# Performance work log

Hardware: AMD Instinct MI355X
Metric: run time of the kernel (lower is better)

The kernel has to match this reference:

```python
import jax, jax.numpy as jnp
import numpy as np

HIDDEN = 1024
N_HEADS = 16
HEAD_DIM = HIDDEN // N_HEADS  # 64; RoPE applied only to first HEAD_DIM channels (head 0)
NUM_BUCKETS = 32
MAX_DISTANCE = 128
MLP_HIDDEN = 4 * HIDDEN
B, N = 2, 2048


def _rotate_half(x):
    # interleaved pairs [a0,b0,a1,b1,...] -> [-b0,a0,-b1,a1,...]
    sh = x.shape
    xr = x.reshape(sh[:-1] + (sh[-1] // 2, 2))
    x1, x2 = xr[..., 0], xr[..., 1]
    return jnp.stack([-x2, x1], axis=-1).reshape(sh)


def _rel_bucket(n, num_buckets=NUM_BUCKETS, max_distance=MAX_DISTANCE):
    # bidirectional T5 bucketing
    ctx = jnp.arange(n)[:, None]
    mem = jnp.arange(n)[None, :]
    rp = mem - ctx  # [n, n]
    nb = num_buckets // 2
    buckets = jnp.where(rp > 0, nb, 0)
    rp = jnp.abs(rp)
    max_exact = nb // 2
    is_small = rp < max_exact
    log_ratio = jnp.log(jnp.maximum(rp, 1).astype(jnp.float32) / max_exact)
    rpl = max_exact + (log_ratio / np.log(max_distance / max_exact) * (nb - max_exact)).astype(jnp.int32)
    rpl = jnp.minimum(rpl, nb - 1)
    return buckets + jnp.where(is_small, rp, rpl)


def _ln(x, eps=1e-6):
    # LayerNorm without affine (DiT elementwise_affine=False)
    m = jnp.mean(x, axis=-1, keepdims=True)
    v = jnp.mean(jnp.square(x - m), axis=-1, keepdims=True)
    return (x - m) * jax.lax.rsqrt(v + eps)


def setup_inputs() -> dict:
    key = jax.random.key(0)
    ks = jax.random.split(key, 12)
    s = 0.02
    return {
        "x": jax.random.normal(ks[0], (B, N, HIDDEN), dtype=jnp.float32),
        "c": jax.random.normal(ks[1], (B, HIDDEN), dtype=jnp.float32),
        "w_ada": jax.random.normal(ks[2], (HIDDEN, 6 * HIDDEN), dtype=jnp.float32) * s,
        "b_ada": jnp.zeros((6 * HIDDEN,), dtype=jnp.float32),
        "w_qkv": jax.random.normal(ks[3], (HIDDEN, 3 * HIDDEN), dtype=jnp.float32) * s,
        "b_qkv": jnp.zeros((3 * HIDDEN,), dtype=jnp.float32),
        "w_out": jax.random.normal(ks[4], (HIDDEN, HIDDEN), dtype=jnp.float32) * s,
        "b_out": jnp.zeros((HIDDEN,), dtype=jnp.float32),
        "rel_table": jax.random.normal(ks[5], (NUM_BUCKETS, N_HEADS), dtype=jnp.float32) * s,
        "w_mlp1": jax.random.normal(ks[6], (HIDDEN, MLP_HIDDEN), dtype=jnp.float32) * s,
        "b_mlp1": jnp.zeros((MLP_HIDDEN,), dtype=jnp.float32),
        "w_mlp2": jax.random.normal(ks[7], (MLP_HIDDEN, HIDDEN), dtype=jnp.float32) * s,
        "b_mlp2": jnp.zeros((HIDDEN,), dtype=jnp.float32),
    }


def reference(x, c, w_ada, b_ada, w_qkv, b_qkv, w_out, b_out, rel_table,
              w_mlp1, b_mlp1, w_mlp2, b_mlp2):
    Bb, n, hid = x.shape
    hd = HEAD_DIM

    # AdaLN-Zero modulation params from conditioning
    mod = jax.nn.silu(c) @ w_ada + b_ada  # [B, 6*hid]
    sh_msa, sc_msa, g_msa, sh_mlp, sc_mlp, g_mlp = jnp.split(mod, 6, axis=-1)

    # --- attention branch ---
    h = _ln(x) * (1.0 + sc_msa[:, None, :]) + sh_msa[:, None, :]
    qkv = h @ w_qkv + b_qkv
    q, k, v = jnp.split(qkv, 3, axis=-1)  # each [B, N, hid]

    # partial RoPE: only first head_dim channels (head 0), interleaved-duplicated freqs
    t = jnp.arange(n, dtype=jnp.float32)
    inv_freq = 1.0 / (10000.0 ** (jnp.arange(0, hd, 2, dtype=jnp.float32) / hd))
    fr = t[:, None] * inv_freq[None, :]               # [N, hd/2]
    fr = jnp.stack([fr, fr], axis=-1).reshape(n, hd)  # [N, hd] interleaved dup
    cos, sin = jnp.cos(fr)[None], jnp.sin(fr)[None]

    def partial_rope(a):
        r, u = a[..., :hd], a[..., hd:]
        r = r * cos + _rotate_half(r) * sin
        return jnp.concatenate([r, u], axis=-1)

    q = partial_rope(q)
    k = partial_rope(k)

    qh = q.reshape(Bb, n, N_HEADS, hd)
    kh = k.reshape(Bb, n, N_HEADS, hd)
    vh = v.reshape(Bb, n, N_HEADS, hd)

    scores = jnp.einsum('bqhd,bkhd->bhqk', qh, kh) / np.float32(np.sqrt(hd))
    bias = rel_table[_rel_bucket(n)]                 # [N, N, H]
    scores = scores + jnp.transpose(bias, (2, 0, 1))[None]  # [1,H,N,N]
    attn = jax.nn.softmax(scores, axis=-1)
    ctxv = jnp.einsum('bhqk,bkhd->bqhd', attn, vh).reshape(Bb, n, hid)
    attn_out = ctxv @ w_out + b_out
    x = x + g_msa[:, None, :] * attn_out

    # --- MLP branch ---
    h2 = _ln(x) * (1.0 + sc_mlp[:, None, :]) + sh_mlp[:, None, :]
    m = jax.nn.gelu(h2 @ w_mlp1 + b_mlp1, approximate=True) @ w_mlp2 + b_mlp2
    return x + g_mlp[:, None, :] * m
```

## Files before the change

kernel.cpp:

```cpp
#include <hip/hip_runtime.h>
#include <hip/hip_bf16.h>

#define SEQ 2048

typedef float f32x4 __attribute__((ext_vector_type(4)));
typedef float f32x16 __attribute__((ext_vector_type(16)));
typedef short short8 __attribute__((ext_vector_type(8)));
typedef int int4v __attribute__((ext_vector_type(4)));

static __device__ __forceinline__ unsigned short f2bf(float f) {
  __hip_bfloat16 h = __float2bfloat16(f);
  unsigned short u;
  __builtin_memcpy(&u, &h, 2);
  return u;
}
static __device__ __forceinline__ float bf2f(unsigned short u) {
  __hip_bfloat16 h;
  __builtin_memcpy(&h, &u, 2);
  return __bfloat162float(h);
}
static __device__ __forceinline__ void gload16(const void* g, void* l) {
  __builtin_amdgcn_global_load_lds(
      (const __attribute__((address_space(1))) void*)g,
      (__attribute__((address_space(3))) void*)l, 16, 0, 0);
}
static __device__ __forceinline__ float gelu_t(float x) {
  float t = x * x;
  float z = x * fmaf(0.1029442695044937f, t, 2.3021181827964594f);
  return x * __builtin_amdgcn_rcpf(1.f + exp2f(-z));
}
static __device__ __forceinline__ unsigned int cvtpk(float lo, float hi) {
  unsigned int r;
  asm("v_cvt_pk_bf16_f32 %0, %1, %2" : "=v"(r) : "v"(lo), "v"(hi));
  return r;
}
static __device__ __forceinline__ void rope_pair(short8& v, int m, int i, float pos) {
  const float fr = exp2f(-(float)(2 * i) * (13.287712379549449f / 64.f));
  const float ang = pos * fr;
  const float sn = sinf(ang), cs = cosf(ang);
  const float x0 = bf2f((unsigned short)v[2 * m]);
  const float x1 = bf2f((unsigned short)v[2 * m + 1]);
  v[2 * m] = (short)f2bf(x0 * cs - x1 * sn);
  v[2 * m + 1] = (short)f2bf(x1 * cs + x0 * sn);
}


#define SOFTMAX_M0 16.0f
__global__ void prep_misc(const float* __restrict__ c, float* __restrict__ siluc,
                          const float* __restrict__ rel_table, float* __restrict__ brp) {
  const int bid = blockIdx.x, t = threadIdx.x;
  if (bid < 8) {
    int i = bid * 256 + t;
    float v = c[i];
    siluc[i] = v / (1.f + expf(-v));
  } else {
    int idx = (bid - 8) * 256 + t;
    int h = idx >> 12, pos = idx & 4095;
    int rp = pos - 2047;
    int bucket = rp > 0 ? 16 : 0;
    int a = rp < 0 ? -rp : rp;
    int bi;
    if (a < 8) {
      bi = a;
    } else {
      bi = 8 + (int)(logf((float)a / 8.f) / 2.772588722239781f * 8.f);
      if (bi > 15) bi = 15;
    }
    brp[idx] = rel_table[(bucket + bi) * 16 + h] * 1.4426950408889634f - SOFTMAX_M0;
  }
}

__global__ void mod_part_k(const float* __restrict__ siluc, const float* __restrict__ w_ada,
                           float* __restrict__ part) {
  int gid = blockIdx.x * 256 + threadIdx.x;
  int kc = gid / 12288;
  int idx = gid - kc * 12288;
  int b = idx / 6144;
  int j = idx - b * 6144;
  const float* cp = siluc + b * 1024 + kc * 64;
  const float* wp = w_ada + (size_t)kc * 64 * 6144 + j;
  float acc = 0.f;
#pragma unroll 8
  for (int k = 0; k < 64; ++k) acc += cp[k] * wp[(size_t)k * 6144];
  part[gid] = acc;
}

__global__ void mod_reduce_k(const float* __restrict__ part, const float* __restrict__ b_ada,
                             float* __restrict__ mod) {
  int idx = blockIdx.x * 256 + threadIdx.x;
  int j = idx % 6144;
  float a = b_ada[j];
#pragma unroll
  for (int kc = 0; kc < 16; ++kc) a += part[kc * 12288 + idx];
  mod[idx] = a;
}

__global__ void transpose_all(const float* __restrict__ w_qkv, const float* __restrict__ w_out,
                              const float* __restrict__ w_mlp1, const float* __restrict__ w_mlp2,
                              unsigned short* __restrict__ dq, unsigned short* __restrict__ dwo,
                              unsigned short* __restrict__ dm1, unsigned short* __restrict__ dm2) {
  __shared__ float tile[32][33];
  const int bid = blockIdx.x;
  const float* src;
  unsigned short* dst;
  int K, N, NT, r;
  if (bid < 3072) {
    src = w_qkv; dst = dq; K = 1024; N = 3072; NT = 96; r = bid;
  } else if (bid < 4096) {
    src = w_out; dst = dwo; K = 1024; N = 1024; NT = 32; r = bid - 3072;
  } else if (bid < 8192) {
    src = w_mlp1; dst = dm1; K = 1024; N = 4096; NT = 128; r = bid - 4096;
  } else {
    src = w_mlp2; dst = dm2; K = 4096; N = 1024; NT = 32; r = bid - 8192;
  }
  const int nt = r % NT, kt = r / NT;
  const int t = threadIdx.x;
  const int col = t & 31, r0 = t >> 5;
#pragma unroll
  for (int i = 0; i < 4; ++i) {
    int rr = r0 + i * 8;
    tile[rr][col] = src[(size_t)(kt * 32 + rr) * N + nt * 32 + col];
  }
  __syncthreads();
#pragma unroll
  for (int i = 0; i < 4; ++i) {
    int rr = r0 + i * 8;
    dst[(size_t)(nt * 32 + rr) * K + kt * 32 + col] = f2bf(tile[col][rr]);
  }
}

__global__ void ln_mod(const float* __restrict__ x, const float* __restrict__ mod,
                       unsigned short* __restrict__ out, int sh_off, int sc_off) {
  int row = blockIdx.x;
  int b = row >> 11;
  int t = threadIdx.x;
  const float4 v = ((const float4*)(x + (size_t)row * 1024))[t];
  float s1 = v.x + v.y + v.z + v.w;
  float s2 = v.x * v.x + v.y * v.y + v.z * v.z + v.w * v.w;
#pragma unroll
  for (int off = 32; off; off >>= 1) {
    s1 += __shfl_xor(s1, off);
    s2 += __shfl_xor(s2, off);
  }
  __shared__ float red[8];
  int w = t >> 6, lane = t & 63;
  if (lane == 0) { red[w] = s1; red[4 + w] = s2; }
  __syncthreads();
  s1 = red[0] + red[1] + red[2] + red[3];
  s2 = red[4] + red[5] + red[6] + red[7];
  float mean = s1 * (1.f / 1024.f);
  float var = s2 * (1.f / 1024.f) - mean * mean;
  float rstd = rsqrtf(var + 1e-6f);
  const float* mb = mod + (size_t)b * 6144;
  int col = t * 4;
  ushort4 o4;
  o4.x = f2bf((v.x - mean) * rstd * (1.f + mb[sc_off + col + 0]) + mb[sh_off + col + 0]);
  o4.y = f2bf((v.y - mean) * rstd * (1.f + mb[sc_off + col + 1]) + mb[sh_off + col + 1]);
  o4.z = f2bf((v.z - mean) * rstd * (1.f + mb[sc_off + col + 2]) + mb[sh_off + col + 2]);
  o4.w = f2bf((v.w - mean) * rstd * (1.f + mb[sc_off + col + 3]) + mb[sh_off + col + 3]);
  *((ushort4*)(out + (size_t)row * 1024 + col)) = o4;
}

__global__ void kvpack(const unsigned short* __restrict__ qkv, unsigned short* __restrict__ kpk,
                       unsigned short* __restrict__ vpk) {
  const int kt = blockIdx.x;
  const int bh = blockIdx.y;
  const int b = bh >> 4, h = bh & 15;
  const int t = threadIdx.x;
  const int s = t >> 6, lane = t & 63;
  const int l31 = lane & 31, hi = lane >> 5;
  const size_t outbase = ((size_t)(bh * 64 + kt) * 4 + s) * 512 + lane * 8;
  {
    const unsigned short* src =
        qkv + (size_t)(b * SEQ + kt * 32 + l31) * 3072 + 1024 + h * 64 + s * 16 + hi * 8;
    short8 kv = *(const short8*)src;
    if (h == 0) {
      const float pos = (float)(kt * 32 + l31);
      const int d0 = s * 16 + hi * 8;
#pragma unroll
      for (int m = 0; m < 4; ++m) rope_pair(kv, m, (d0 >> 1) + m, pos);
    }
    *(short8*)(kpk + outbase) = kv;
  }
  {
    const int krow = kt * 32 + (s & 1) * 16 + hi * 8;
    const int d = (s >> 1) * 32 + l31;
    const unsigned short* src = qkv + (size_t)(b * SEQ + krow) * 3072 + 2048 + h * 64 + d;
    unsigned short v[8];
#pragma unroll
    for (int j = 0; j < 8; ++j) v[j] = src[(size_t)j * 3072];
    *(short8*)(vpk + outbase) = *(const short8*)v;
  }
}

template <int MODE, int BM, int BN, int PIPE>
__global__ __launch_bounds__(256) void gemm_bt(
    const unsigned short* __restrict__ A, const unsigned short* __restrict__ Bt,
    const float* __restrict__ bias, void* __restrict__ outp, const float* __restrict__ res,
    const float* __restrict__ mod, int goff, int N, int K) {
  constexpr int NBUF = PIPE ? 2 : 1;
  __shared__ __align__(16) unsigned short a_lds[NBUF][BM * 64];
  __shared__ __align__(16) unsigned short b_lds[NBUF][BN * 64];
  constexpr int WM = BM / 2, WN = BN / 2;
  constexpr int MT = WM / 16, NT = WN / 16;
  const int t = threadIdx.x;
  const int lane = t & 63;
  const int l15 = lane & 15, l4 = lane >> 4;
  const int w = t >> 6;
  const int wr = w >> 1, wc = w & 1;
  const int gx = gridDim.x;
  const int nwg = gx * gridDim.y;
  int wg = blockIdx.y * gx + blockIdx.x;
  wg = (wg & 7) * (nwg >> 3) + (wg >> 3);
  const int by = wg / gx, bx = wg - by * gx;
  const int rowA0 = by * BM;
  const int rowB0 = bx * BN;
  const int wub = t & ~63;

  f32x4 acc[MT][NT];
#pragma unroll
  for (int m = 0; m < MT; ++m)
#pragma unroll
    for (int n = 0; n < NT; ++n) acc[m][n] = (f32x4){0.f, 0.f, 0.f, 0.f};

  auto stage = [&](int buf, int kt) {
#pragma unroll
    for (int rnd = 0; rnd < BM / 32; ++rnd) {
      const int idx = rnd * 256 + t;
      const int row = idx >> 3;
      const int cb = ((idx & 7) << 4) ^ ((row & 7) << 4);
      const char* sa = (const char*)(A + (size_t)(rowA0 + row) * K + kt) + cb;
      gload16(sa, (char*)(&a_lds[buf][0]) + (size_t)(rnd * 256 + wub) * 16);
    }
#pragma unroll
    for (int rnd = 0; rnd < BN / 32; ++rnd) {
      const int idx = rnd * 256 + t;
      const int row = idx >> 3;
      const int cb = ((idx & 7) << 4) ^ ((row & 7) << 4);
      const char* sb = (const char*)(Bt + (size_t)(rowB0 + row) * K + kt) + cb;
      gload16(sb, (char*)(&b_lds[buf][0]) + (size_t)(rnd * 256 + wub) * 16);
    }
  };

  auto compute = [&](int buf) {
#pragma unroll
    for (int kb = 0; kb < 2; ++kb) {
      short8 af[MT], bfr[NT];
#pragma unroll
      for (int m = 0; m < MT; ++m) {
        int row = wr * WM + m * 16 + l15;
        int cb = (kb * 64 + l4 * 16) ^ ((row & 7) << 4);
        af[m] = *(const short8*)((const char*)(&a_lds[buf][0]) + row * 128 + cb);
      }
#pragma unroll
      for (int n = 0; n < NT; ++n) {
        int row = wc * WN + n * 16 + l15;
        int cb = (kb * 64 + l4 * 16) ^ ((row & 7) << 4);
        bfr[n] = *(const short8*)((const char*)(&b_lds[buf][0]) + row * 128 + cb);
      }
      __builtin_amdgcn_s_setprio(1);
#pragma unroll
      for (int m = 0; m < MT; ++m)
#pragma unroll
        for (int n = 0; n < NT; ++n)
          acc[m][n] = __builtin_amdgcn_mfma_f32_16x16x32_bf16(af[m], bfr[n], acc[m][n], 0, 0, 0);
      __builtin_amdgcn_s_setprio(0);
    }
  };

  if (PIPE) {
    stage(0, 0);
    __syncthreads();
    int cur = 0;
    for (int kt = 0; kt < K; kt += 64) {
      if (kt + 64 < K) stage(cur ^ 1, kt + 64);
      compute(cur);
      __syncthreads();
      cur ^= 1;
    }
  } else {
    for (int kt = 0; kt < K; kt += 64) {
      stage(0, kt);
      __syncthreads();
      compute(0);
      __syncthreads();
    }
  }

#pragma unroll
  for (int n = 0; n < NT; ++n) {
    const int col = rowB0 + wc * WN + n * 16 + l15;
    const float bv = bias[col];
#pragma unroll
    for (int m = 0; m < MT; ++m) {
      const int row0 = rowA0 + wr * WM + m * 16 + l4 * 4;
#pragma unroll
      for (int r = 0; r < 4; ++r) {
        float v = acc[m][n][r] + bv;
        const size_t o = (size_t)(row0 + r) * N + col;
        if (MODE == 0) {
          ((unsigned short*)outp)[o] = f2bf(v);
        } else if (MODE == 1) {
          ((unsigned short*)outp)[o] = f2bf(gelu_t(v));
        } else {
          float g = mod[(size_t)((row0 + r) >> 11) * 6144 + goff + col];
          ((float*)outp)[o] = res[o] + g * v;
        }
      }
    }
  }
}

__global__ __launch_bounds__(256) void attn_k(const unsigned short* __restrict__ qkv,
                                              const unsigned short* __restrict__ kpk,
                                              const unsigned short* __restrict__ vpk,
                                              const float* __restrict__ brp_all,
                                              unsigned short* __restrict__ ctxv) {
  const int t = threadIdx.x;
  const int w = t >> 6;
  const int lane = t & 63;
  const int l31 = lane & 31;
  const int hi = lane >> 5;
  const int wg = blockIdx.x;
  const int xcd = wg & 7, idx = wg >> 3;
  const int bh = xcd * 4 + (idx >> 4);
  const int qt = idx & 15;
  const int b = bh >> 4, h = bh & 15;
  const int qw = qt * 128 + w * 32;
  const float SC = 0.125f * 1.4426950408889634f;
  const float* brp = brp_all + (size_t)h * 4096;

  short8 qfr[4];
  {
    const unsigned short* qrow = qkv + (size_t)(b * SEQ + qw + l31) * 3072 + h * 64 + hi * 8;
#pragma unroll
    for (int kk = 0; kk < 4; ++kk) qfr[kk] = *(const short8*)(qrow + kk * 16);
    if (h == 0) {
      const float pos = (float)(qw + l31);
#pragma unroll
      for (int kk = 0; kk < 4; ++kk) {
        const int d0 = kk * 16 + hi * 8;
#pragma unroll
        for (int m = 0; m < 4; ++m) rope_pair(qfr[kk], m, (d0 >> 1) + m, pos);
      }
    }
  }
  const float bfar_pos = brp[4095], bfar_neg = brp[0];
  const float* bql = brp + 2047 + 4 * hi - (qw + l31);

  short8 ones;
#pragma unroll
  for (int i = 0; i < 8; ++i) ones[i] = (short)0x3F80;

  const unsigned short* kp = kpk + ((size_t)(bh * 64)) * 2048 + lane * 8;
  const unsigned short* vp = vpk + ((size_t)(bh * 64)) * 2048 + lane * 8;

  short8 kfrA[4], vfrA[4], kfrB[4], vfrB[4];
#pragma unroll
  for (int s = 0; s < 4; ++s) {
    kfrA[s] = *(const short8*)(kp + s * 512);
    vfrA[s] = *(const short8*)(vp + s * 512);
  }
  kp += 2048;
  vp += 2048;

  f32x16 oacc0 = {}, oacc1 = {}, lacc = {};
  int kbase = 0;

#define ATTN_TILE(KF, VF, KFN, VFN)                                                       \
  do {                                                                                    \
    KFN[0] = *(const short8*)(kp);                                                        \
    KFN[1] = *(const short8*)(kp + 512);                                                  \
    KFN[2] = *(const short8*)(kp + 1024);                                                 \
    KFN[3] = *(const short8*)(kp + 1536);                                                 \
    VFN[0] = *(const short8*)(vp);                                                        \
    VFN[1] = *(const short8*)(vp + 512);                                                  \
    VFN[2] = *(const short8*)(vp + 1024);                                                 \
    VFN[3] = *(const short8*)(vp + 1536);                                                 \
    kp += 2048;                                                                           \
    vp += 2048;                                                                           \
    f32x16 sacc = {};                                                                     \
    sacc = __builtin_amdgcn_mfma_f32_32x32x16_bf16(KF[0], qfr[0], sacc, 0, 0, 0);         \
    sacc = __builtin_amdgcn_mfma_f32_32x32x16_bf16(KF[1], qfr[1], sacc, 0, 0, 0);         \
    sacc = __builtin_amdgcn_mfma_f32_32x32x16_bf16(KF[2], qfr[2], sacc, 0, 0, 0);         \
    sacc = __builtin_amdgcn_mfma_f32_32x32x16_bf16(KF[3], qfr[3], sacc, 0, 0, 0);         \
    float p[16];                                                                          \
    const int dd = kbase - qw;                                                            \
    if (dd >= 128 || dd <= -128) {                                                        \
      const float bf_ = (dd > 0) ? bfar_pos : bfar_neg;                                   \
      _Pragma("unroll") for (int r = 0; r < 16; ++r)                                      \
          p[r] = __builtin_amdgcn_exp2f(fmaf(sacc[r], SC, bf_));                          \
    } else {                                                                              \
      const float* bp = bql + kbase;                                                      \
      _Pragma("unroll") for (int r = 0; r < 16; ++r)                                      \
          p[r] = __builtin_amdgcn_exp2f(fmaf(sacc[r], SC, bp[(r & 3) + 8 * (r >> 2)]));   \
    }                                                                                     \
    unsigned int x0 = cvtpk(p[0], p[1]), x1 = cvtpk(p[2], p[3]);                          \
    unsigned int y0 = cvtpk(p[4], p[5]), y1 = cvtpk(p[6], p[7]);                          \
    asm("v_permlane32_swap_b32 %0, %1" : "+v"(x0), "+v"(y0));                             \
    asm("v_permlane32_swap_b32 %0, %1" : "+v"(x1), "+v"(y1));                             \
    unsigned int x2 = cvtpk(p[8], p[9]), x3 = cvtpk(p[10], p[11]);                        \
    unsigned int y2 = cvtpk(p[12], p[13]), y3 = cvtpk(p[14], p[15]);                      \
    asm("v_permlane32_swap_b32 %0, %1" : "+v"(x2), "+v"(y2));                             \
    asm("v_permlane32_swap_b32 %0, %1" : "+v"(x3), "+v"(y3));                             \
    int4v pi0 = {(int)x0, (int)x1, (int)y0, (int)y1};                                     \
    int4v pi1 = {(int)x2, (int)x3, (int)y2, (int)y3};                                     \
    short8 pf0 = __builtin_bit_cast(short8, pi0);                                         \
    short8 pf1 = __builtin_bit_cast(short8, pi1);                                         \
    lacc = __builtin_amdgcn_mfma_f32_32x32x16_bf16(ones, pf0, lacc, 0, 0, 0);             \
    lacc = __builtin_amdgcn_mfma_f32_32x32x16_bf16(ones, pf1, lacc, 0, 0, 0);             \
    oacc0 = __builtin_amdgcn_mfma_f32_32x32x16_bf16(VF[0], pf0, oacc0, 0, 0, 0);          \
    oacc0 = __builtin_amdgcn_mfma_f32_32x32x16_bf16(VF[1], pf1, oacc0, 0, 0, 0);          \
    oacc1 = __builtin_amdgcn_mfma_f32_32x32x16_bf16(VF[2], pf0, oacc1, 0, 0, 0);          \
    oacc1 = __builtin_amdgcn_mfma_f32_32x32x16_bf16(VF[3], pf1, oacc1, 0, 0, 0);          \
    kbase += 32;                                                                          \
  } while (0)

#pragma unroll 1
  for (int it = 0; it < 32; ++it) {
    ATTN_TILE(kfrA, vfrA, kfrB, vfrB);
    ATTN_TILE(kfrB, vfrB, kfrA, vfrA);
  }
#undef ATTN_TILE

  const float inv = 1.f / lacc[0];
  unsigned short* orow = ctxv + (size_t)(b * SEQ + qw + l31) * 1024 + h * 64;
#pragma unroll
  for (int r = 0; r < 16; r += 2) {
    const int d = (r & 3) + 8 * (r >> 2) + 4 * hi;
    *(unsigned int*)(orow + d) = cvtpk(oacc0[r] * inv, oacc0[r + 1] * inv);
    *(unsigned int*)(orow + 32 + d) = cvtpk(oacc1[r] * inv, oacc1[r + 1] * inv);
  }
}

extern "C" void kernel_launch(void* const* d_in, const int* in_sizes, int n_in, void* d_out,
                              int out_size, void* d_ws, size_t ws_size, hipStream_t stream) {
  (void)in_sizes; (void)n_in; (void)out_size; (void)ws_size;
  const float* x = (const float*)d_in[0];
  const float* c = (const float*)d_in[1];
  const float* w_ada = (const float*)d_in[2];
  const float* b_ada = (const float*)d_in[3];
  const float* w_qkv = (const float*)d_in[4];
  const float* b_qkv = (const float*)d_in[5];
  const float* w_out = (const float*)d_in[6];
  const float* b_out = (const float*)d_in[7];
  const float* rel_t = (const float*)d_in[8];
  const float* w_mlp1 = (const float*)d_in[9];
  const float* b_mlp1 = (const float*)d_in[10];
  const float* w_mlp2 = (const float*)d_in[11];
  const float* b_mlp2 = (const float*)d_in[12];
  float* out = (float*)d_out;
  char* ws = (char*)d_ws;

  constexpr size_t OFF_WQKVT = 0;
  constexpr size_t OFF_WOUTT = OFF_WQKVT + (size_t)3072 * 1024 * 2;
  constexpr size_t OFF_WM1T = OFF_WOUTT + (size_t)1024 * 1024 * 2;
  constexpr size_t OFF_WM2T = OFF_WM1T + (size_t)4096 * 1024 * 2;
  constexpr size_t OFF_H = OFF_WM2T + (size_t)1024 * 4096 * 2;
  constexpr size_t OFF_QKV = OFF_H + (size_t)4096 * 1024 * 2;
  constexpr size_t OFF_VT = OFF_QKV + (size_t)4096 * 3072 * 2;
  constexpr size_t OFF_CTXV = OFF_VT + (size_t)32 * 64 * 2048 * 2;
  constexpr size_t OFF_MID = OFF_CTXV + (size_t)4096 * 1024 * 2;
  constexpr size_t OFF_SILU = OFF_MID + (size_t)4096 * 4096 * 2;
  constexpr size_t OFF_MOD = OFF_SILU + 2048 * 4;
  constexpr size_t OFF_BRP = OFF_MOD + 12288 * 4;
  constexpr size_t OFF_PART = OFF_BRP + 65536 * 4;

  unsigned short* wqkvT = (unsigned short*)(ws + OFF_WQKVT);
  unsigned short* woutT = (unsigned short*)(ws + OFF_WOUTT);
  unsigned short* wm1T = (unsigned short*)(ws + OFF_WM1T);
  unsigned short* wm2T = (unsigned short*)(ws + OFF_WM2T);
  unsigned short* hbuf = (unsigned short*)(ws + OFF_H);
  unsigned short* qkvbuf = (unsigned short*)(ws + OFF_QKV);
  unsigned short* vpkbuf = (unsigned short*)(ws + OFF_VT);
  unsigned short* ctxvbuf = (unsigned short*)(ws + OFF_CTXV);
  unsigned short* midbuf = (unsigned short*)(ws + OFF_MID);
  unsigned short* kpkbuf = (unsigned short*)(ws + OFF_MID);
  float* siluc = (float*)(ws + OFF_SILU);
  float* modb = (float*)(ws + OFF_MOD);
  float* brp = (float*)(ws + OFF_BRP);
  float* part = (float*)(ws + OFF_PART);

  prep_misc<<<264, 256, 0, stream>>>(c, siluc, rel_t, brp);
  mod_part_k<<<768, 256, 0, stream>>>(siluc, w_ada, part);
  mod_reduce_k<<<48, 256, 0, stream>>>(part, b_ada, modb);
  transpose_all<<<12288, 256, 0, stream>>>(w_qkv, w_out, w_mlp1, w_mlp2, wqkvT, woutT, wm1T,
                                           wm2T);

  ln_mod<<<4096, 256, 0, stream>>>(x, modb, hbuf, 0, 1024);
  gemm_bt<0, 128, 128, 0><<<dim3(24, 32), 256, 0, stream>>>(hbuf, wqkvT, b_qkv, qkvbuf, nullptr,
                                                            nullptr, 0, 3072, 1024);
  kvpack<<<dim3(64, 32), 256, 0, stream>>>(qkvbuf, kpkbuf, vpkbuf);
  attn_k<<<512, 256, 0, stream>>>(qkvbuf, kpkbuf, vpkbuf, brp, ctxvbuf);
  gemm_bt<2, 64, 64, 1><<<dim3(16, 64), 256, 0, stream>>>(ctxvbuf, woutT, b_out, out, x, modb,
                                                          2048, 1024, 1024);
  ln_mod<<<4096, 256, 0, stream>>>(out, modb, hbuf, 3072, 4096);
  gemm_bt<1, 128, 128, 0><<<dim3(32, 32), 256, 0, stream>>>(hbuf, wm1T, b_mlp1, midbuf, nullptr,
                                                            nullptr, 0, 4096, 1024);
  gemm_bt<2, 64, 64, 1><<<dim3(16, 64), 256, 0, stream>>>(midbuf, wm2T, b_mlp2, out, out, modb,
                                                          5120, 1024, 4096);
}
```

Baseline: 255.5 us.

## Fuse K/V packing into QKV GEMM epilogue and merge prep kernels

The QKV GEMM gets a new epilogue mode that scatters K and V directly into the packed attention layouts, so the separate kvpack kernel no longer re-reads the QKV buffer. RoPE on head 0 of K is applied by a small in-place krope_fix kernel. The prep_misc and transpose_all kernels are merged into one launch to save a kernel launch. The cost is scattered, uncoalesced 2-byte stores in the GEMM epilogue, which may slow that GEMM.

```diff
diff --git a/kernel.cpp b/kernel.cpp
--- a/kernel.cpp
+++ b/kernel.cpp
@@ -46,27 +46,62 @@
 
 
 #define SOFTMAX_M0 16.0f
-__global__ void prep_misc(const float* __restrict__ c, float* __restrict__ siluc,
-                          const float* __restrict__ rel_table, float* __restrict__ brp) {
-  const int bid = blockIdx.x, t = threadIdx.x;
-  if (bid < 8) {
-    int i = bid * 256 + t;
-    float v = c[i];
-    siluc[i] = v / (1.f + expf(-v));
+__global__ void prep_transpose(const float* __restrict__ w_qkv, const float* __restrict__ w_out,
+                               const float* __restrict__ w_mlp1, const float* __restrict__ w_mlp2,
+                               unsigned short* __restrict__ dq, unsigned short* __restrict__ dwo,
+                               unsigned short* __restrict__ dm1, unsigned short* __restrict__ dm2,
+                               const float* __restrict__ c, float* __restrict__ siluc,
+                               const float* __restrict__ rel_table, float* __restrict__ brp) {
+  const int bid = blockIdx.x;
+  const int t = threadIdx.x;
+  if (bid >= 12288) {
+    const int pb = bid - 12288;
+    if (pb < 8) {
+      int i = pb * 256 + t;
+      float v = c[i];
+      siluc[i] = v / (1.f + expf(-v));
+    } else {
+      int idx = (pb - 8) * 256 + t;
+      int h = idx >> 12, pos = idx & 4095;
+      int rp = pos - 2047;
+      int bucket = rp > 0 ? 16 : 0;
+      int a = rp < 0 ? -rp : rp;
+      int bi;
+      if (a < 8) {
+        bi = a;
+      } else {
+        bi = 8 + (int)(logf((float)a / 8.f) / 2.772588722239781f * 8.f);
+        if (bi > 15) bi = 15;
+      }
+      brp[idx] = rel_table[(bucket + bi) * 16 + h] * 1.4426950408889634f - SOFTMAX_M0;
+    }
+    return;
+  }
+  __shared__ float tile[32][33];
+  const float* src;
+  unsigned short* dst;
+  int K, N, NT, r;
+  if (bid < 3072) {
+    src = w_qkv; dst = dq; K = 1024; N = 3072; NT = 96; r = bid;
+  } else if (bid < 4096) {
+    src = w_out; dst = dwo; K = 1024; N = 1024; NT = 32; r = bid - 3072;
+  } else if (bid < 8192) {
+    src = w_mlp1; dst = dm1; K = 1024; N = 4096; NT = 128; r = bid - 4096;
   } else {
-    int idx = (bid - 8) * 256 + t;
-    int h = idx >> 12, pos = idx & 4095;
-    int rp = pos - 2047;
-    int bucket = rp > 0 ? 16 : 0;
-    int a = rp < 0 ? -rp : rp;
-    int bi;
-    if (a < 8) {
-      bi = a;
-    } else {
-      bi = 8 + (int)(logf((float)a / 8.f) / 2.772588722239781f * 8.f);
-      if (bi > 15) bi = 15;
-    }
-    brp[idx] = rel_table[(bucket + bi) * 16 + h] * 1.4426950408889634f - SOFTMAX_M0;
+    src = w_mlp2; dst = dm2; K = 4096; N = 1024; NT = 32; r = bid - 8192;
+  }
+  const int nt = r % NT, kt = r / NT;
+  const int col = t & 31, r0 = t >> 5;
+#pragma unroll
+  for (int i = 0; i < 4; ++i) {
+    int rr = r0 + i * 8;
+    tile[rr][col] = src[(size_t)(kt * 32 + rr) * N + nt * 32 + col];
+  }
+  __syncthreads();
+#pragma unroll
+  for (int i = 0; i < 4; ++i) {
+    int rr = r0 + i * 8;
+    dst[(size_t)(nt * 32 + rr) * K + kt * 32 + col] = f2bf(tile[col][rr]);
   }
 }
 
@@ -93,40 +128,6 @@
 #pragma unroll
   for (int kc = 0; kc < 16; ++kc) a += part[kc * 12288 + idx];
   mod[idx] = a;
-}
-
-__global__ void transpose_all(const float* __restrict__ w_qkv, const float* __restrict__ w_out,
-                              const float* __restrict__ w_mlp1, const float* __restrict__ w_mlp2,
-                              unsigned short* __restrict__ dq, unsigned short* __restrict__ dwo,
-                              unsigned short* __restrict__ dm1, unsigned short* __restrict__ dm2) {
-  __shared__ float tile[32][33];
-  const int bid = blockIdx.x;
-  const float* src;
-  unsigned short* dst;
-  int K, N, NT, r;
-  if (bid < 3072) {
-    src = w_qkv; dst = dq; K = 1024; N = 3072; NT = 96; r = bid;
-  } else if (bid < 4096) {
-    src = w_out; dst = dwo; K = 1024; N = 1024; NT = 32; r = bid - 3072;
-  } else if (bid < 8192) {
-    src = w_mlp1; dst = dm1; K = 1024; N = 4096; NT = 128; r = bid - 4096;
-  } else {
-    src = w_mlp2; dst = dm2; K = 4096; N = 1024; NT = 32; r = bid - 8192;
-  }
-  const int nt = r % NT, kt = r / NT;
-  const int t = threadIdx.x;
-  const int col = t & 31, r0 = t >> 5;
-#pragma unroll
-  for (int i = 0; i < 4; ++i) {
-    int rr = r0 + i * 8;
-    tile[rr][col] = src[(size_t)(kt * 32 + rr) * N + nt * 32 + col];
-  }
-  __syncthreads();
-#pragma unroll
-  for (int i = 0; i < 4; ++i) {
-    int rr = r0 + i * 8;
-    dst[(size_t)(nt * 32 + rr) * K + kt * 32 + col] = f2bf(tile[col][rr]);
-  }
 }
 
 __global__ void ln_mod(const float* __restrict__ x, const float* __restrict__ mod,
@@ -161,43 +162,32 @@
   *((ushort4*)(out + (size_t)row * 1024 + col)) = o4;
 }
 
-__global__ void kvpack(const unsigned short* __restrict__ qkv, unsigned short* __restrict__ kpk,
-                       unsigned short* __restrict__ vpk) {
-  const int kt = blockIdx.x;
-  const int bh = blockIdx.y;
-  const int b = bh >> 4, h = bh & 15;
-  const int t = threadIdx.x;
-  const int s = t >> 6, lane = t & 63;
-  const int l31 = lane & 31, hi = lane >> 5;
-  const size_t outbase = ((size_t)(bh * 64 + kt) * 4 + s) * 512 + lane * 8;
-  {
-    const unsigned short* src =
-        qkv + (size_t)(b * SEQ + kt * 32 + l31) * 3072 + 1024 + h * 64 + s * 16 + hi * 8;
-    short8 kv = *(const short8*)src;
-    if (h == 0) {
-      const float pos = (float)(kt * 32 + l31);
-      const int d0 = s * 16 + hi * 8;
-#pragma unroll
-      for (int m = 0; m < 4; ++m) rope_pair(kv, m, (d0 >> 1) + m, pos);
-    }
-    *(short8*)(kpk + outbase) = kv;
-  }
-  {
-    const int krow = kt * 32 + (s & 1) * 16 + hi * 8;
-    const int d = (s >> 1) * 32 + l31;
-    const unsigned short* src = qkv + (size_t)(b * SEQ + krow) * 3072 + 2048 + h * 64 + d;
-    unsigned short v[8];
-#pragma unroll
-    for (int j = 0; j < 8; ++j) v[j] = src[(size_t)j * 3072];
-    *(short8*)(vpk + outbase) = *(const short8*)v;
-  }
+__global__ void krope_fix(unsigned short* __restrict__ kpk) {
+  const int gid = blockIdx.x * 256 + threadIdx.x;
+  const int i = gid & 31;
+  const int l31 = (gid >> 5) & 31;
+  const int kt = (gid >> 10) & 63;
+  const int b = gid >> 16;
+  const int d = 2 * i;
+  const int bh = b * 16;
+  const size_t addr = (((size_t)(bh * 64 + kt) * 4 + (d >> 4)) * 512) +
+                      (((d >> 3) & 1) * 32 + l31) * 8 + (d & 7);
+  unsigned int pv = *(unsigned int*)(kpk + addr);
+  const float x0 = bf2f((unsigned short)(pv & 0xFFFF));
+  const float x1 = bf2f((unsigned short)(pv >> 16));
+  const float fr = exp2f(-(float)d * (13.287712379549449f / 64.f));
+  const float ang = (float)(kt * 32 + l31) * fr;
+  const float sn = sinf(ang), cs = cosf(ang);
+  *(unsigned int*)(kpk + addr) =
+      (unsigned int)f2bf(x0 * cs - x1 * sn) | ((unsigned int)f2bf(x1 * cs + x0 * sn) << 16);
 }
 
 template <int MODE, int BM, int BN, int PIPE>
 __global__ __launch_bounds__(256) void gemm_bt(
     const unsigned short* __restrict__ A, const unsigned short* __restrict__ Bt,
     const float* __restrict__ bias, void* __restrict__ outp, const float* __restrict__ res,
-    const float* __restrict__ mod, int goff, int N, int K) {
+    const float* __restrict__ mod, int goff, int N, int K,
+    unsigned short* __restrict__ kpkp, unsigned short* __restrict__ vpkp) {
   constexpr int NBUF = PIPE ? 2 : 1;
   __shared__ __align__(16) unsigned short a_lds[NBUF][BM * 64];
   __shared__ __align__(16) unsigned short b_lds[NBUF][BN * 64];
@@ -297,14 +287,37 @@
 #pragma unroll
       for (int r = 0; r < 4; ++r) {
         float v = acc[m][n][r] + bv;
-        const size_t o = (size_t)(row0 + r) * N + col;
         if (MODE == 0) {
-          ((unsigned short*)outp)[o] = f2bf(v);
+          ((unsigned short*)outp)[(size_t)(row0 + r) * N + col] = f2bf(v);
         } else if (MODE == 1) {
-          ((unsigned short*)outp)[o] = f2bf(gelu_t(v));
-        } else {
+          ((unsigned short*)outp)[(size_t)(row0 + r) * N + col] = f2bf(gelu_t(v));
+        } else if (MODE == 2) {
+          const size_t o = (size_t)(row0 + r) * N + col;
           float g = mod[(size_t)((row0 + r) >> 11) * 6144 + goff + col];
           ((float*)outp)[o] = res[o] + g * v;
+        } else {
+          const int rr = row0 + r;
+          if (rowB0 < 1024) {
+            ((unsigned short*)outp)[(size_t)rr * N + col] = f2bf(v);
+          } else if (rowB0 < 2048) {
+            const int bb = rr >> 11, krow = rr & 2047;
+            const int colk = col - 1024;
+            const int hh = colk >> 6, d = colk & 63;
+            const int bh2 = bb * 16 + hh;
+            const size_t addr = (((size_t)(bh2 * 64 + (krow >> 5)) * 4 + (d >> 4)) * 512) +
+                                (((d >> 3) & 1) * 32 + (krow & 31)) * 8 + (d & 7);
+            kpkp[addr] = f2bf(v);
+          } else {
+            const int bb = rr >> 11, krow = rr & 2047;
+            const int colv = col - 2048;
+            const int hh = colv >> 6, d = colv & 63;
+            const int bh2 = bb * 16 + hh;
+            const int r5 = krow & 31;
+            const int f = (d >> 5) * 2 + (r5 >> 4);
+            const size_t addr = (((size_t)(bh2 * 64 + (krow >> 5)) * 4 + f) * 512) +
+                                (((r5 >> 3) & 1) * 32 + (d & 31)) * 8 + (r5 & 7);
+            vpkp[addr] = f2bf(v);
+          }
         }
       }
     }
@@ -481,22 +494,23 @@
   float* brp = (float*)(ws + OFF_BRP);
   float* part = (float*)(ws + OFF_PART);
 
-  prep_misc<<<264, 256, 0, stream>>>(c, siluc, rel_t, brp);
+  prep_transpose<<<12552, 256, 0, stream>>>(w_qkv, w_out, w_mlp1, w_mlp2, wqkvT, woutT, wm1T,
+                                            wm2T, c, siluc, rel_t, brp);
   mod_part_k<<<768, 256, 0, stream>>>(siluc, w_ada, part);
   mod_reduce_k<<<48, 256, 0, stream>>>(part, b_ada, modb);
-  transpose_all<<<12288, 256, 0, stream>>>(w_qkv, w_out, w_mlp1, w_mlp2, wqkvT, woutT, wm1T,
-                                           wm2T);
 
   ln_mod<<<4096, 256, 0, stream>>>(x, modb, hbuf, 0, 1024);
-  gemm_bt<0, 128, 128, 0><<<dim3(24, 32), 256, 0, stream>>>(hbuf, wqkvT, b_qkv, qkvbuf, nullptr,
-                                                            nullptr, 0, 3072, 1024);
-  kvpack<<<dim3(64, 32), 256, 0, stream>>>(qkvbuf, kpkbuf, vpkbuf);
+  gemm_bt<3, 128, 128, 0><<<dim3(24, 32), 256, 0, stream>>>(hbuf, wqkvT, b_qkv, qkvbuf, nullptr,
+                                                            nullptr, 0, 3072, 1024, kpkbuf,
+                                                            vpkbuf);
+  krope_fix<<<512, 256, 0, stream>>>(kpkbuf);
   attn_k<<<512, 256, 0, stream>>>(qkvbuf, kpkbuf, vpkbuf, brp, ctxvbuf);
   gemm_bt<2, 64, 64, 1><<<dim3(16, 64), 256, 0, stream>>>(ctxvbuf, woutT, b_out, out, x, modb,
-                                                          2048, 1024, 1024);
+                                                          2048, 1024, 1024, nullptr, nullptr);
   ln_mod<<<4096, 256, 0, stream>>>(out, modb, hbuf, 3072, 4096);
   gemm_bt<1, 128, 128, 0><<<dim3(32, 32), 256, 0, stream>>>(hbuf, wm1T, b_mlp1, midbuf, nullptr,
-                                                            nullptr, 0, 4096, 1024);
+                                                            nullptr, 0, 4096, 1024, nullptr,
+                                                            nullptr);
   gemm_bt<2, 64, 64, 1><<<dim3(16, 64), 256, 0, stream>>>(midbuf, wm2T, b_mlp2, out, out, modb,
-                                                          5120, 1024, 4096);
-}
+                                                          5120, 1024, 4096, nullptr, nullptr);
+}
```

New measurement: 238.7 us (median of 2 runs). 1.07x faster.
